# Optimization experiments

Hardware: AMD Instinct MI355X
Metric: run time of the kernel (lower is better)

## Reference

```python
import jax, jax.numpy as jnp
import numpy as np

L = 48                 # lattice side
M = 2 * L * L          # 4608 spin-orbitals (spinful: 2 per site)
N_OCC = 1024           # occupied fermions
N_HID = 24             # hidden fermions
NT2 = 2 * N_HID        # pairing channels in CNN output
JASTROW = 16
CH = NT2 + JASTROW     # 64 CNN channels
NBLOCKS = 4
K = 3                  # conv kernel size


def conv2d_circular(x, w, b):
    # x: (C,H,W), w: (O,I,K,K); 'SAME' conv with circular (periodic) padding
    p = K // 2
    xp = jnp.pad(x, ((0, 0), (p, p), (p, p)), mode='wrap')
    y = jax.lax.conv_general_dilated(xp[None], w, (1, 1), 'VALID',
                                     dimension_numbers=('NCHW', 'OIHW', 'NCHW'))[0]
    if b is not None:
        y = y + b[:, None, None]
    return y


def cnn_forward(x, params):
    # ReshapeConv: flat spinful config (M,) -> (2, L, L)
    h = x.reshape(2, L, L)
    for i, (w1, b1, w2, b2) in enumerate(params):
        res = h
        t = h / jnp.sqrt(i + 1.0)
        t = t / jnp.sqrt(2.0) if i == 0 else jax.nn.gelu(t)
        t = jax.nn.gelu(conv2d_circular(t, w1, b1))
        t = conv2d_circular(t, w2, b2)
        if t.shape[0] > res.shape[0]:
            res = jnp.repeat(res, t.shape[0] // res.shape[0], axis=0)
        h = t + res
    return h / jnp.sqrt(NBLOCKS + 1.0)


def pfaffian_sign(A):
    # Sign of the Pfaffian of skew-symmetric A via Householder tridiagonalization.
    # pf(A) = det(Q) * prod(superdiag of T over even positions); det(Q)=(-1)^{#reflections}.
    n = A.shape[0]
    idx = jnp.arange(n)

    def body(k, carry):
        A, ds = carry
        col = A[:, k]
        xv = jnp.where(idx > k, col, 0.0)
        normx = jnp.sqrt(jnp.sum(xv * xv))
        s = jnp.where(col[k + 1] >= 0, 1.0, -1.0)
        v = xv - (-s * normx) * (idx == k + 1).astype(A.dtype)
        vn = jnp.sqrt(jnp.sum(v * v))
        ok = vn > 1e-30
        v = jnp.where(ok, v / jnp.where(ok, vn, 1.0), 0.0)
        u = A @ v
        # H A H for skew A with H = I - 2 v v^T  (v^T A v = 0)
        A = A + 2.0 * jnp.outer(v, u) - 2.0 * jnp.outer(u, v)
        return A, jnp.where(ok, -ds, ds)

    A, ds = jax.lax.fori_loop(0, n - 2, body, (A, jnp.array(1.0, A.dtype)))
    sup = jnp.diagonal(A, offset=1)[::2]
    return ds * jnp.prod(jnp.sign(sup))


def setup_inputs() -> dict:
    key = jax.random.key(0)
    ks = jax.random.split(key, 32)
    # occupation config in {+1,-1} with exactly N_OCC occupied modes
    occ = jnp.concatenate([jnp.ones(N_OCC, jnp.float32), -jnp.ones(M - N_OCC, jnp.float32)])
    x = jax.random.permutation(ks[0], occ)

    def he(k, shape):
        fan_in = shape[1] * shape[2] * shape[3]
        return jax.random.normal(k, shape, jnp.float32) * jnp.sqrt(2.0 / fan_in)

    inp = {
        'x': x,
        'F_vv': jax.random.normal(ks[1], (M, M), jnp.float32),
        'F_hh': jax.random.normal(ks[2], (N_HID, N_HID), jnp.float32),
    }
    j = 3
    for b in range(NBLOCKS):
        cin = 2 if b == 0 else CH
        inp[f'w1_{b}'] = he(ks[j], (CH, cin, K, K)); j += 1
        inp[f'b1_{b}'] = jnp.zeros((CH,), jnp.float32)
        inp[f'w2_{b}'] = he(ks[j], (CH, CH, K, K)); j += 1
        if b < NBLOCKS - 1:  # last block conv2 has no bias
            inp[f'b2_{b}'] = jnp.zeros((CH,), jnp.float32)
    return inp


def reference(x, F_vv, F_hh,
              w1_0, b1_0, w2_0, b2_0,
              w1_1, b1_1, w2_1, b2_1,
              w1_2, b1_2, w2_2, b2_2,
              w1_3, b1_3, w2_3):
    params = [(w1_0, b1_0, w2_0, b2_0),
              (w1_1, b1_1, w2_1, b2_1),
              (w1_2, b1_2, w2_2, b2_2),
              (w1_3, b1_3, w2_3, None)]
    out = cnn_forward(x, params)                     # (CH, L, L)
    n = jnp.nonzero(x == 1, size=N_OCC)[0]           # occupied mode indices
    log_J = out[NT2:].sum()                          # Jastrow log-factor (real)
    F_vh = out[:NT2].reshape(-1, M).T                # (M, N_HID)
    Fvv = 0.5 * (F_vv - F_vv.T)
    Fvh_n = F_vh[n]                                  # (N_OCC, N_HID)
    A = jnp.block([[Fvv[n][:, n], Fvh_n],
                   [-Fvh_n.T, 0.5 * (F_hh - F_hh.T)]])  # (N_OCC+N_HID,)^2 skew
    sign = pfaffian_sign(jax.lax.stop_gradient(A))   # cos(angle(sign)) == sign for real dtype
    logabspf = 0.5 * jnp.linalg.slogdet(A)[1]        # |pf(A)| = sqrt(|det(A)|)
    return sign, logabspf + log_J
```

## Files before the change

kernel.cpp:

```cpp
#include <hip/hip_runtime.h>
#include <math.h>


#define NPIX 2304
#define MSZ  4608
#define NOCC 1024
#define NHID 24
#define PF_N 1048
#define PF_BLOCKS 256
#define NPAN 17

__device__ __forceinline__ float gelu_f(float v){
  float v3 = v*v*v;
  return 0.5f*v*(1.0f + tanhf(0.7978845608028654f*(v + 0.044715f*v3)));
}

__device__ __forceinline__ void ast(double* p, double v){
  __hip_atomic_store(p, v, __ATOMIC_RELAXED, __HIP_MEMORY_SCOPE_AGENT);
}

__global__ void k_prep(const float* __restrict__ x, int* __restrict__ nidx,
                       float* __restrict__ tbuf){
  __shared__ int cnt[256];
  __shared__ int off[256];
  int t = threadIdx.x;
  int c = 0;
  for (int k = 0; k < 18; k++){
    int idx = t*18 + k;
    float v = x[idx];
    c += (v == 1.0f) ? 1 : 0;
    tbuf[idx] = v * 0.70710678118654752f;
  }
  cnt[t] = c;
  __syncthreads();
  if (t == 0){ int s = 0; for (int q=0;q<256;q++){ off[q]=s; s+=cnt[q]; } }
  __syncthreads();
  int o = off[t];
  for (int k = 0; k < 18; k++){
    int idx = t*18+k;
    if (x[idx] == 1.0f) nidx[o++] = idx;
  }
}

__global__ __launch_bounds__(128) void k_conv(const float* __restrict__ in,
      const float* __restrict__ wgt, const float* __restrict__ bias,
      const float* __restrict__ res, float* __restrict__ outp,
      float* __restrict__ pre_out, double* __restrict__ logJ_acc,
      int cin, int resmode, int dogelu, float scale, float pre_scale){
  const int c  = blockIdx.x / 6;
  const int rg = blockIdx.x % 6;
  const int tid = threadIdx.x;
  const int y  = rg*8 + (tid >> 4);
  const int xg = (tid & 15)*3;
  const int ym = ((y+47)%48)*48, y0 = y*48, yp = ((y+1)%48)*48;
  int c5[5];
  #pragma unroll
  for (int t = 0; t < 5; t++){
    int xx = xg - 1 + t;
    c5[t] = (xx < 0) ? 47 : ((xx >= 48) ? xx - 48 : xx);
  }
  float s0 = 0.f, s1 = 0.f, s2 = 0.f;
  const float* wp = wgt + c*cin*9;
  for (int ci = 0; ci < cin; ci++){
    const float* b_ = in + ci*NPIX;
    #pragma unroll
    for (int rr = 0; rr < 3; rr++){
      const int rb = (rr == 0) ? ym : ((rr == 1) ? y0 : yp);
      float v0 = b_[rb+c5[0]], v1 = b_[rb+c5[1]], v2 = b_[rb+c5[2]];
      float v3 = b_[rb+c5[3]], v4 = b_[rb+c5[4]];
      float w0 = wp[3*rr], w1 = wp[3*rr+1], w2 = wp[3*rr+2];
      s0 += v0*w0 + v1*w1 + v2*w2;
      s1 += v1*w0 + v2*w1 + v3*w2;
      s2 += v2*w0 + v3*w1 + v4*w2;
    }
    wp += 9;
  }
  const float bv = bias ? bias[c] : 0.f;
  const int base = c*NPIX + y0 + xg;
  float sv[3] = {s0, s1, s2};
  double ls = 0.0;
  #pragma unroll
  for (int t = 0; t < 3; t++){
    float s = sv[t] + bv;
    if (dogelu) s = gelu_f(s);
    if (resmode == 1) s += res[c*NPIX + y0 + xg + t];
    else if (resmode == 2) s += res[(c>>5)*NPIX + y0 + xg + t];
    s *= scale;
    outp[base+t] = s;
    if (pre_out) pre_out[base+t] = gelu_f(s * pre_scale);
    ls += (double)s;
  }
  if (logJ_acc && c >= 48){
    for (int o = 32; o > 0; o >>= 1) ls += __shfl_down(ls, o, 64);
    if ((tid & 63) == 0) atomicAdd(logJ_acc, ls);
  }
}

__global__ __launch_bounds__(256) void k_buildAvv(const float* __restrict__ Fvv,
      const int* __restrict__ nidx, double* __restrict__ A){
  __shared__ float G1[32][33], G2[32][33];
  __shared__ int sNi[32], sNj[32];
  int I = 0, item = blockIdx.x;
  while ((I+1)*(I+2)/2 <= item) I++;
  const int J = item - I*(I+1)/2;
  const int i0 = I*32, j0 = J*32;
  const int tid = threadIdx.x;
  if (tid < 32){ sNi[tid] = nidx[i0+tid]; }
  else if (tid < 64){ sNj[tid-32] = nidx[j0+tid-32]; }
  __syncthreads();
  for (int idx = tid; idx < 32*32; idx += 256){
    const int r = idx >> 5, c = idx & 31;
    G1[r][c] = Fvv[(size_t)sNi[r]*MSZ + sNj[c]];
    G2[r][c] = Fvv[(size_t)sNj[r]*MSZ + sNi[c]];
  }
  __syncthreads();
  for (int idx = tid; idx < 32*32; idx += 256){
    const int r = idx >> 5, c = idx & 31;
    const int i = i0 + r, j = j0 + c;
    if (i > j)
      A[(size_t)i*PF_N + j] = 0.5*((double)G1[r][c] - (double)G2[c][r]);
  }
}

__global__ void k_buildAs(const float* __restrict__ Fhh,
      const float* __restrict__ hfin, const int* __restrict__ nidx,
      double* __restrict__ A){
  int g = blockIdx.x*256 + threadIdx.x;
  if (g >= 24*PF_N) return;
  const int i = NOCC + g / PF_N, j = g % PF_N;
  if (j >= i) return;
  const int r = i - NOCC;
  double v;
  if (j < NOCC){
    int nj = nidx[j];
    int ss = (nj >= NPIX) ? 1 : 0;
    v = -(double)hfin[(2*r+ss)*NPIX + (nj - ss*NPIX)];
  } else {
    int r2 = j - NOCC;
    v = 0.5*((double)Fhh[r*NHID + r2] - (double)Fhh[r2*NHID + r]);
  }
  A[(size_t)i*PF_N + j] = v;
}

__device__ __forceinline__ void gridbar(unsigned* flags, unsigned ep){
  __syncthreads();
  const int tid = threadIdx.x;
  if (tid == 0){
    asm volatile("" ::: "memory");
    __builtin_amdgcn_s_waitcnt(0);
    __hip_atomic_store(&flags[blockIdx.x], ep, __ATOMIC_RELAXED,
                       __HIP_MEMORY_SCOPE_AGENT);
  }
  if (tid < 64){
    for (;;){
      unsigned v0 = __hip_atomic_load(&flags[tid      ], __ATOMIC_RELAXED, __HIP_MEMORY_SCOPE_AGENT);
      unsigned v1 = __hip_atomic_load(&flags[tid +  64], __ATOMIC_RELAXED, __HIP_MEMORY_SCOPE_AGENT);
      unsigned v2 = __hip_atomic_load(&flags[tid + 128], __ATOMIC_RELAXED, __HIP_MEMORY_SCOPE_AGENT);
      unsigned v3 = __hip_atomic_load(&flags[tid + 192], __ATOMIC_RELAXED, __HIP_MEMORY_SCOPE_AGENT);
      bool ok = (v0 >= ep) & (v1 >= ep) & (v2 >= ep) & (v3 >= ep);
      if (__all(ok)) break;
      __builtin_amdgcn_s_sleep(1);
    }
    asm volatile("" ::: "memory");
  }
  __syncthreads();
}

__device__ __forceinline__ size_t pk_off(int k){
  return (size_t)64 * ((size_t)984*(size_t)k - (size_t)32*(size_t)k*(size_t)(k-1));
}

__global__ __launch_bounds__(256) void k_pf(const double* __restrict__ A,
      double* __restrict__ Pbase, double* __restrict__ Dbase,
      unsigned* __restrict__ flags, const double* __restrict__ logJ,
      float* __restrict__ outp){
  const int N = PF_N;
  const int tid = threadIdx.x;
  const int b = blockIdx.x;
  const int nrows = (b < 24) ? 5 : 4;

  __shared__ double rowbuf[2688];
  __shared__ double Dt[64*65];
  __shared__ double sAA[32][64];
  __shared__ double sBB[32][64];
  __shared__ double sInvL[32], sTf[32];
  __shared__ double sCA[5][32], sCB[5][32];

  #define RIDX(s)  (b + 256*(s))
  #define ROFF(s)  ((s)*b + 128*(s)*((s)-1))

  for (int s = 0; s < nrows; s++){
    const int i = RIDX(s);
    const int o = ROFF(s);
    const double* Ar = A + (size_t)i*N;
    for (int j = tid; j < i; j += 256) rowbuf[o+j] = Ar[j];
  }
  __syncthreads();

  if (b < 64){
    for (int c = tid; c < b; c += 256)
      ast(&Dbase[(size_t)b*64 + c], rowbuf[c]);
  }
  unsigned ep = 0;
  gridbar(flags, ++ep);

  double lsum = 0.0; int nneg = 0;

  for (int k = 0; k < NPAN; k++){
    const int c0  = 64*k;
    const int w   = (N - c0 < 64) ? (N - c0) : 64;
    const int np  = w >> 1;
    const int tc0 = c0 + w;
    const int m   = N - tc0;
    const double* Dk = Dbase + (size_t)k*4096;
    double* Pk = Pbase + pk_off(k);

    {
      for (int idx = tid; idx < 64*64; idx += 256){
        int r = idx >> 6, c = idx & 63;
        if (r > c && r < w) Dt[r*65+c] = Dk[r*64+c];
      }
      __syncthreads();
      const int r = tid & 63, qu = tid >> 6;
      for (int j = 0; j < np; j++){
        const int r0 = 2*j, r1 = r0 + 1;
        const double t = -Dt[r1*65 + r0];
        const double invt = 1.0 / t;
        if (tid == 0){ sTf[j] = t; sInvL[j] = invt; }
        const bool rowok = (r < w) && (r >= r0 + 2);
        if (rowok){
          const double ar = Dt[r*65 + r0], br = Dt[r*65 + r1];
          if (qu == 0){ sAA[j][r] = ar * invt; sBB[j][r] = br * invt; }
          const int lo = r0 + 2, hi = r;
          const int per = (hi - lo + 3) >> 2;
          const int cb = lo + qu*per;
          int ce = cb + per; if (ce > hi) ce = hi;
          for (int c = cb; c < ce; c++){
            const double ac = Dt[c*65 + r0], bc = Dt[c*65 + r1];
            Dt[r*65 + c] += (br*ac - ar*bc) * invt;
          }
        }
        __syncthreads();
      }
      if (b == 0 && tid < 64){
        double lv = 0.0; int sg = 0;
        if (tid < np){ double t = sTf[tid]; lv = log(fabs(t)); sg = (t<0.0)?1:0; }
        for (int o = 32; o > 0; o >>= 1){
          lv += __shfl_down(lv, o, 64);
          sg += __shfl_down(sg, o, 64);
        }
        if (tid == 0){ lsum += lv; nneg += sg; }
      }
    }

    if (m > 0){
      const int wv = tid >> 6, lc = tid & 63;
      for (int s = wv; s < nrows; s += 4){
        const int i = RIDX(s);
        if (i < tc0) continue;
        const int o = ROFF(s);
        double v = rowbuf[o + c0 + lc];
        #pragma unroll 8
        for (int j = 0; j < 32; j++){
          double a  = __shfl(v, 2*j,   64);
          double bb = __shfl(v, 2*j+1, 64);
          if (lc >= 2*j+2) v += bb*sAA[j][lc] - a*sBB[j][lc];
        }
        rowbuf[o + c0 + lc] = v;
        ast(&Pk[(size_t)(i - tc0)*64 + lc], v);
      }
      __syncthreads();
      {
        const int s = tid >> 5, l = tid & 31;
        if (tid < 160 && s < nrows){
          const int i = RIDX(s);
          if (i >= tc0){
            const int o = ROFF(s);
            sCA[s][l] = rowbuf[o + c0 + 2*l    ] * sInvL[l];
            sCB[s][l] = rowbuf[o + c0 + 2*l + 1] * sInvL[l];
          }
        }
      }
    }
    gridbar(flags, ++ep);

    if (m > 0){
      const int maxOwn = RIDX(nrows-1);
      for (int base = tc0; base < maxOwn; base += 256){
        const int j = base + tid;
        const bool jv = (j < maxOwn);
        double acc[5];
        #pragma unroll
        for (int s = 0; s < 5; s++){
          acc[s] = 0.0;
          if (s < nrows && jv && j < RIDX(s)) acc[s] = rowbuf[ROFF(s) + j];
        }
        if (jv){
          const double* pr = Pk + (size_t)(j - tc0)*64;
          #pragma unroll 4
          for (int l = 0; l < 32; l++){
            double a  = pr[2*l];
            double bb = pr[2*l+1];
            #pragma unroll
            for (int s = 0; s < 5; s++)
              acc[s] += sCB[s][l]*a - sCA[s][l]*bb;
          }
          #pragma unroll
          for (int s = 0; s < 5; s++)
            if (s < nrows && j < RIDX(s)) rowbuf[ROFF(s) + j] = acc[s];
        }
      }
      __syncthreads();
      for (int s = 0; s < nrows; s++){
        const int i = RIDX(s);
        if (i >= tc0 && i < tc0 + 64){
          double* Dn = Dbase + (size_t)(k+1)*4096 + (size_t)(i - tc0)*64;
          const int o = ROFF(s);
          for (int c = tid; c < i - tc0; c += 256)
            ast(&Dn[c], rowbuf[o + tc0 + c]);
        }
      }
    }
    gridbar(flags, ++ep);
  }

  if (b == 0 && tid == 0){
    outp[0] = (nneg & 1) ? -1.0f : 1.0f;
    outp[1] = (float)(lsum + logJ[0]);
  }
  #undef RIDX
  #undef ROFF
}

extern "C" void kernel_launch(void* const* d_in, const int* in_sizes, int n_in,
                              void* d_out, int out_size, void* d_ws, size_t ws_size,
                              hipStream_t stream){
  (void)in_sizes; (void)n_in; (void)out_size; (void)ws_size;
  const float* x   = (const float*)d_in[0];
  const float* Fvv = (const float*)d_in[1];
  const float* Fhh = (const float*)d_in[2];
  const float* w1[4] = {(const float*)d_in[3], (const float*)d_in[7],
                        (const float*)d_in[11], (const float*)d_in[15]};
  const float* b1[4] = {(const float*)d_in[4], (const float*)d_in[8],
                        (const float*)d_in[12], (const float*)d_in[16]};
  const float* w2[4] = {(const float*)d_in[5], (const float*)d_in[9],
                        (const float*)d_in[13], (const float*)d_in[17]};
  const float* b2[3] = {(const float*)d_in[6], (const float*)d_in[10],
                        (const float*)d_in[14]};

  char* ws = (char*)d_ws;
  unsigned* flags = (unsigned*)(ws + 0);
  double* logJa   = (double*)(ws + 1024);
  int*    nidx    = (int*)(ws + 1088);
  const size_t CB = 589824;
  float* tbuf  = (float*)(ws + 74240);
  float* ybuf  = (float*)(ws + 74240 + CB);
  float* hbuf0 = (float*)(ws + 74240 + 2*CB);
  float* hbuf1 = (float*)(ws + 74240 + 3*CB);
  double* A     = (double*)(ws + 2433536);
  double* Pbase = (double*)(ws + 11220992);
  double* Dbase = (double*)(ws + 15349760);

  hipMemsetAsync(d_ws, 0, 2048, stream);
  k_prep<<<1,256,0,stream>>>(x, nidx, tbuf);

  k_conv<<<384,128,0,stream>>>(tbuf, w1[0], b1[0], nullptr, ybuf,
                               nullptr, nullptr, 2, 0, 1, 1.0f, 0.f);
  k_conv<<<384,128,0,stream>>>(ybuf, w2[0], b2[0], x, hbuf0,
                               tbuf, nullptr, 64, 2, 0, 1.0f,
                               0.70710678118654752f);
  k_conv<<<384,128,0,stream>>>(tbuf, w1[1], b1[1], nullptr, ybuf,
                               nullptr, nullptr, 64, 0, 1, 1.0f, 0.f);
  k_conv<<<384,128,0,stream>>>(ybuf, w2[1], b2[1], hbuf0, hbuf1,
                               tbuf, nullptr, 64, 1, 0, 1.0f,
                               0.57735026918962576f);
  k_conv<<<384,128,0,stream>>>(tbuf, w1[2], b1[2], nullptr, ybuf,
                               nullptr, nullptr, 64, 0, 1, 1.0f, 0.f);
  k_conv<<<384,128,0,stream>>>(ybuf, w2[2], b2[2], hbuf1, hbuf0,
                               tbuf, nullptr, 64, 1, 0, 1.0f, 0.5f);
  k_conv<<<384,128,0,stream>>>(tbuf, w1[3], b1[3], nullptr, ybuf,
                               nullptr, nullptr, 64, 0, 1, 1.0f, 0.f);
  k_conv<<<384,128,0,stream>>>(ybuf, w2[3], nullptr, hbuf0, hbuf1,
                               nullptr, logJa, 64, 1, 0,
                               0.44721359549995794f, 0.f);

  k_buildAvv<<<528,256,0,stream>>>(Fvv, nidx, A);
  k_buildAs<<<(24*PF_N+255)/256,256,0,stream>>>(Fhh, hbuf1, nidx, A);

  k_pf<<<PF_BLOCKS,256,0,stream>>>(A, Pbase, Dbase, flags, logJa,
                                   (float*)d_out);
}
```

Baseline: 1.170 ms.

## Drop sAA/sBB shared tables, restructure panel update loop, vectorize P loads

Removes the sAA/sBB shared arrays (32 KB of LDS) and recomputes the scaled panel entries from Dt and sInvL when rows are updated, which lowers LDS use per block. The in-panel elimination now uses a fixed 16-column unrolled slice per thread with the column values preloaded into registers, replacing the variable-length inner loop. The trailing update reads P rows as double2 with full unrolling. This trades extra LDS reads and multiplies, plus more register pressure, for fewer shared allocations and better load vectorization.

```diff
diff --git a/kernel.cpp b/kernel.cpp
--- a/kernel.cpp
+++ b/kernel.cpp
@@ -181,8 +181,6 @@
 
   __shared__ double rowbuf[2688];
   __shared__ double Dt[64*65];
-  __shared__ double sAA[32][64];
-  __shared__ double sBB[32][64];
   __shared__ double sInvL[32], sTf[32];
   __shared__ double sCA[5][32], sCB[5][32];
 
@@ -217,28 +215,33 @@
 
     {
       for (int idx = tid; idx < 64*64; idx += 256){
-        int r = idx >> 6, c = idx & 63;
-        if (r > c && r < w) Dt[r*65+c] = Dk[r*64+c];
+        int r_ = idx >> 6, c_ = idx & 63;
+        if (r_ > c_ && r_ < w) Dt[r_*65+c_] = Dk[r_*64+c_];
       }
       __syncthreads();
-      const int r = tid & 63, qu = tid >> 6;
+      const int r_ = tid & 63, qu = tid >> 6;
       for (int j = 0; j < np; j++){
         const int r0 = 2*j, r1 = r0 + 1;
         const double t = -Dt[r1*65 + r0];
         const double invt = 1.0 / t;
         if (tid == 0){ sTf[j] = t; sInvL[j] = invt; }
-        const bool rowok = (r < w) && (r >= r0 + 2);
-        if (rowok){
-          const double ar = Dt[r*65 + r0], br = Dt[r*65 + r1];
-          if (qu == 0){ sAA[j][r] = ar * invt; sBB[j][r] = br * invt; }
-          const int lo = r0 + 2, hi = r;
-          const int per = (hi - lo + 3) >> 2;
-          const int cb = lo + qu*per;
-          int ce = cb + per; if (ce > hi) ce = hi;
-          for (int c = cb; c < ce; c++){
-            const double ac = Dt[c*65 + r0], bc = Dt[c*65 + r1];
-            Dt[r*65 + c] += (br*ac - ar*bc) * invt;
-          }
+        const bool rowok = (r_ < w) && (r_ >= r0 + 2);
+        const int cb = r0 + 2 + qu*16;
+        double ac[16], bc[16];
+        #pragma unroll
+        for (int u = 0; u < 16; u++){
+          const int c_ = cb + u;
+          const int cc = (c_ < w) ? c_ : (w-1);
+          ac[u] = Dt[cc*65 + r0];
+          bc[u] = Dt[cc*65 + r1];
+        }
+        double ar = 0.0, br = 0.0;
+        if (rowok){ ar = Dt[r_*65 + r0]; br = Dt[r_*65 + r1]; }
+        #pragma unroll
+        for (int u = 0; u < 16; u++){
+          const int c_ = cb + u;
+          if (rowok && c_ < r_)
+            Dt[r_*65 + c_] += (br*ac[u] - ar*bc[u]) * invt;
         }
         __syncthreads();
       }
@@ -264,7 +267,12 @@
         for (int j = 0; j < 32; j++){
           double a  = __shfl(v, 2*j,   64);
           double bb = __shfl(v, 2*j+1, 64);
-          if (lc >= 2*j+2) v += bb*sAA[j][lc] - a*sBB[j][lc];
+          if (lc >= 2*j+2){
+            const double it = sInvL[j];
+            const double ha = Dt[lc*65 + 2*j    ] * it;
+            const double hb = Dt[lc*65 + 2*j + 1] * it;
+            v += bb*ha - a*hb;
+          }
         }
         rowbuf[o + c0 + lc] = v;
         ast(&Pk[(size_t)(i - tc0)*64 + lc], v);
@@ -296,14 +304,13 @@
           if (s < nrows && jv && j < RIDX(s)) acc[s] = rowbuf[ROFF(s) + j];
         }
         if (jv){
-          const double* pr = Pk + (size_t)(j - tc0)*64;
-          #pragma unroll 4
+          const double2* pr2 = (const double2*)(Pk + (size_t)(j - tc0)*64);
+          #pragma unroll
           for (int l = 0; l < 32; l++){
-            double a  = pr[2*l];
-            double bb = pr[2*l+1];
+            const double2 ab = pr2[l];
             #pragma unroll
             for (int s = 0; s < 5; s++)
-              acc[s] += sCB[s][l]*a - sCA[s][l]*bb;
+              acc[s] += sCB[s][l]*ab.x - sCA[s][l]*ab.y;
           }
           #pragma unroll
           for (int s = 0; s < 5; s++)
```

Result: slower. 2.211 ms (+89.0%).
